# Performance work log

Hardware: AMD Instinct MI355X
Metric: run time of the kernel (lower is better)

Reference implementation:

```python
import jax, jax.numpy as jnp
import numpy as np

B, N, D = 4, 4096, 2048
E = D // 2  # inter_channels of the non-local block


def setup_inputs() -> dict:
    key = jax.random.key(0)
    ks = jax.random.split(key, 9)
    s_in = 1.0 / np.sqrt(D)   # conv1d(k=1) default init scale, fan_in=D
    s_e = 1.0 / np.sqrt(E)    # W conv: fan_in=E
    return {
        "images_feat": jax.random.normal(ks[0], (B, N, D), jnp.float32),
        "theta_w": jax.random.uniform(ks[1], (E, D), jnp.float32, -s_in, s_in),
        "theta_b": jax.random.uniform(ks[2], (E,), jnp.float32, -s_in, s_in),
        "phi_w": jax.random.uniform(ks[3], (E, D), jnp.float32, -s_in, s_in),
        "phi_b": jax.random.uniform(ks[4], (E,), jnp.float32, -s_in, s_in),
        "g_w": jax.random.uniform(ks[5], (E, D), jnp.float32, -s_in, s_in),
        "g_b": jax.random.uniform(ks[6], (E,), jnp.float32, -s_in, s_in),
        "W_w": jax.random.uniform(ks[7], (D, E), jnp.float32, -s_e, s_e),
        "W_b": jax.random.uniform(ks[8], (D,), jnp.float32, -s_e, s_e),
    }


def reference(images_feat, theta_w, theta_b, phi_w, phi_b, g_w, g_b, W_w, W_b):
    # Original: permute (B,N,D)->(B,D,N), apply 1x1 Conv1d projections (== linear
    # over the channel dim D), theta@phi^T -> softmax -> @g, W conv back, residual,
    # permute back. Expressed directly on (B,N,D).
    x = images_feat
    theta_x = jnp.einsum("bnd,ed->bne", x, theta_w) + theta_b  # (B,N,E)
    phi_x = jnp.einsum("bnd,ed->bne", x, phi_w) + phi_b        # (B,N,E)
    g_x = jnp.einsum("bnd,ed->bne", x, g_w) + g_b              # (B,N,E)
    f = jnp.einsum("bne,bme->bnm", theta_x, phi_x)             # (B,N,N)
    attn = jax.nn.softmax(f, axis=-1)
    y = jnp.einsum("bnm,bme->bne", attn, g_x)                  # (B,N,E)
    z = jnp.einsum("bne,de->bnd", y, W_w) + W_b + x            # residual, (B,N,D)
    return z
```

## Files before the change

### kernel.cpp

```cpp
#include <hip/hip_runtime.h>

typedef short bf16x8 __attribute__((ext_vector_type(8)));
typedef _Float16 f16x8 __attribute__((ext_vector_type(8)));
typedef float f32x4 __attribute__((ext_vector_type(4)));

__device__ __forceinline__ short f2h(float f) {
  _Float16 h = (_Float16)f;
  return __builtin_bit_cast(short, h);
}
__device__ __forceinline__ float h2f(short s) {
  return (float)__builtin_bit_cast(_Float16, s);
}

__device__ __forceinline__ void gload16(const void* g, void* lds) {
  __builtin_amdgcn_global_load_lds(
      (const __attribute__((address_space(1))) unsigned*)g,
      (__attribute__((address_space(3))) unsigned*)lds, 16, 0, 0);
}

template <int NF, int K, int OMODE, int BIAS_MODE, int RES>
__global__ __launch_bounds__(512, 2) void gemm256(
    const short* __restrict__ A, int lda, long sA,
    const short* __restrict__ B, int ldb, long sB,
    void* __restrict__ Cv, int ldc, long sC,
    const float* __restrict__ bias, const float* __restrict__ resid, long sR) {
  constexpr int BN = NF * 64;
  constexpr int BNB = BN * 128;
  constexpr int NT = K / 64;
  __shared__ char lds[65536 + 2 * BNB];

  A += (size_t)blockIdx.z * sA;
  B += (size_t)blockIdx.z * sB;
  char* Cb = (char*)Cv + (size_t)blockIdx.z * sC * (OMODE == 0 ? 4 : 2);
  const float* res = resid ? resid + (size_t)blockIdx.z * sR : nullptr;

  const int tid = threadIdx.x;
  const int wid = tid >> 6, lane = tid & 63;
  const int wr = wid >> 2, wc = wid & 3;
  const int fr = lane & 15, fq = lane >> 4;
  const size_t bm = (size_t)blockIdx.y * 256;
  const size_t bn = (size_t)blockIdx.x * BN;

  const int srow = wid * 8 + (lane >> 3);
  const int scolS = ((lane & 7) * 16) ^ ((srow & 7) << 4);
  const char* Ag = (const char*)A;
  const char* Bg = (const char*)B;

  const int swz = (fr & 7) << 4;
  int aoff[8], boff[NF];
#pragma unroll
  for (int m = 0; m < 8; m++)
    aoff[m] = (wr * 128 + m * 16 + fr) * 128 + ((fq * 16) ^ swz);
#pragma unroll
  for (int n = 0; n < NF; n++)
    boff[n] = (wc * NF * 16 + n * 16 + fr) * 128 + ((fq * 16) ^ swz);

  f32x4 acc[8][NF];
#pragma unroll
  for (int m = 0; m < 8; m++)
#pragma unroll
    for (int n = 0; n < NF; n++) acc[m][n] = (f32x4){0.f, 0.f, 0.f, 0.f};

  auto stage = [&](int t, int d) {
    const int ktb = t * 128;
#pragma unroll
    for (int c = 0; c < 4; ++c)
      gload16(Ag + ((size_t)(bm + c * 64 + srow) * lda) * 2 + ktb + scolS,
              &lds[d * 32768 + c * 8192 + wid * 1024]);
#pragma unroll
    for (int c = 0; c < NF; ++c)
      gload16(Bg + ((size_t)(bn + c * 64 + srow) * ldb) * 2 + ktb + scolS,
              &lds[65536 + d * BNB + c * 8192 + wid * 1024]);
  };

  stage(0, 0);
  int cur = 0;
#pragma unroll 2
  for (int t = 0; t < NT; ++t) {
    if (t + 1 < NT) stage(t + 1, cur ^ 1);
    __builtin_amdgcn_sched_barrier(0);
    if (t + 1 < NT) {
      if constexpr (NF == 4)
        asm volatile("s_waitcnt vmcnt(8)");
      else
        asm volatile("s_waitcnt vmcnt(6)");
    } else {
      asm volatile("s_waitcnt vmcnt(0)");
    }
    __builtin_amdgcn_sched_barrier(0);
    __builtin_amdgcn_s_barrier();
    __builtin_amdgcn_sched_barrier(0);
    {
      const int dA = cur * 32768, dB = 65536 + cur * BNB;
#pragma unroll
      for (int ks = 0; ks < 2; ++ks) {
        f16x8 ar[8], br[NF];
#pragma unroll
        for (int m = 0; m < 8; m++)
          ar[m] = *(const f16x8*)&lds[dA + (aoff[m] ^ (ks << 6))];
#pragma unroll
        for (int n = 0; n < NF; n++)
          br[n] = *(const f16x8*)&lds[dB + (boff[n] ^ (ks << 6))];
#pragma unroll
        for (int m = 0; m < 8; m++)
#pragma unroll
          for (int n = 0; n < NF; n++)
            acc[m][n] = __builtin_amdgcn_mfma_f32_16x16x32_f16(
                ar[m], br[n], acc[m][n], 0, 0, 0);
      }
    }
    __builtin_amdgcn_sched_barrier(0);
    __builtin_amdgcn_s_barrier();
    __builtin_amdgcn_sched_barrier(0);
    cur ^= 1;
  }

#pragma unroll
  for (int m = 0; m < 8; m++) {
    const size_t row0 = bm + wr * 128 + m * 16 + fq * 4;
#pragma unroll
    for (int n = 0; n < NF; n++) {
      const size_t col = bn + wc * NF * 16 + n * 16 + fr;
      float bcol = (BIAS_MODE == 1) ? bias[col] : 0.f;
#pragma unroll
      for (int r = 0; r < 4; r++) {
        float val = acc[m][n][r];
        const size_t row = row0 + r;
        const size_t idx = row * (size_t)ldc + col;
        if (BIAS_MODE == 1) val += bcol;
        if (BIAS_MODE == 2) val += bias[row];
        if (RES) val += res[idx];
        if (OMODE == 0)
          ((float*)Cb)[idx] = val;
        else
          ((short*)Cb)[idx] = f2h(val);
      }
    }
  }
}

__global__ __launch_bounds__(256) void cvt_f32_f16(const float* __restrict__ s,
                                                   short* __restrict__ d, int n) {
  int i = (blockIdx.x * 256 + threadIdx.x) * 8;
  if (i >= n) return;
  const float4 a = *(const float4*)(s + i);
  const float4 b = *(const float4*)(s + i + 4);
  bf16x8 o;
  o[0] = f2h(a.x); o[1] = f2h(a.y); o[2] = f2h(a.z); o[3] = f2h(a.w);
  o[4] = f2h(b.x); o[5] = f2h(b.y); o[6] = f2h(b.z); o[7] = f2h(b.w);
  *(bf16x8*)(d + i) = o;
}

__global__ __launch_bounds__(256) void softmax_rows(short* __restrict__ S) {
  const size_t row = blockIdx.x;
  short* rp = S + row * 4096;
  const int tid = threadIdx.x;
  const int lane = tid & 63, wid = tid >> 6;
  float v[16];
#pragma unroll
  for (int c = 0; c < 2; c++) {
    bf16x8 xv = *(const bf16x8*)(rp + (c * 256 + tid) * 8);
#pragma unroll
    for (int j = 0; j < 8; j++) v[c * 8 + j] = h2f(xv[j]);
  }
  float m = v[0];
#pragma unroll
  for (int i = 1; i < 16; i++) m = fmaxf(m, v[i]);
#pragma unroll
  for (int off = 32; off >= 1; off >>= 1) m = fmaxf(m, __shfl_xor(m, off));
  __shared__ float red[8];
  if (lane == 0) red[wid] = m;
  __syncthreads();
  m = fmaxf(fmaxf(red[0], red[1]), fmaxf(red[2], red[3]));
  float s = 0.f;
#pragma unroll
  for (int i = 0; i < 16; i++) {
    v[i] = __expf(v[i] - m);
    s += v[i];
  }
#pragma unroll
  for (int off = 32; off >= 1; off >>= 1) s += __shfl_xor(s, off);
  if (lane == 0) red[4 + wid] = s;
  __syncthreads();
  s = (red[4] + red[5]) + (red[6] + red[7]);
  const float rs = 1.0f / s;
#pragma unroll
  for (int c = 0; c < 2; c++) {
    bf16x8 o;
#pragma unroll
    for (int j = 0; j < 8; j++) o[j] = f2h(v[c * 8 + j] * rs);
    *(bf16x8*)(rp + (c * 256 + tid) * 8) = o;
  }
}

extern "C" void kernel_launch(void* const* d_in, const int* in_sizes, int n_in,
                              void* d_out, int out_size, void* d_ws,
                              size_t ws_size, hipStream_t stream) {
  const float* x   = (const float*)d_in[0];
  const float* thw = (const float*)d_in[1];
  const float* thb = (const float*)d_in[2];
  const float* phw = (const float*)d_in[3];
  const float* phb = (const float*)d_in[4];
  const float* gw  = (const float*)d_in[5];
  const float* gbi = (const float*)d_in[6];
  const float* Ww  = (const float*)d_in[7];
  const float* Wb  = (const float*)d_in[8];
  float* out = (float*)d_out;

  char* ws = (char*)d_ws;
  short* xf   = (short*)(ws);
  short* wcat = (short*)(ws + 67108864);
  short* gwb  = (short*)(ws + 75497472);
  short* wWb  = (short*)(ws + 79691776);
  float* bc   = (float*)(ws + 83886080);
  short* tpf  = (short*)(ws + 83894272);
  short* gT   = (short*)(ws + 151003136);
  short* sc   = (short*)(ws);

  cvt_f32_f16<<<16384, 256, 0, stream>>>(x, xf, 33554432);
  cvt_f32_f16<<<1024, 256, 0, stream>>>(thw, wcat, 2097152);
  cvt_f32_f16<<<1024, 256, 0, stream>>>(phw, wcat + 2097152, 2097152);
  cvt_f32_f16<<<1024, 256, 0, stream>>>(gw, gwb, 2097152);
  cvt_f32_f16<<<1024, 256, 0, stream>>>(Ww, wWb, 2097152);
  hipMemcpyAsync(bc, thb, 4096, hipMemcpyDeviceToDevice, stream);
  hipMemcpyAsync(bc + 1024, phb, 4096, hipMemcpyDeviceToDevice, stream);

  gemm256<4, 2048, 1, 1, 0><<<dim3(8, 64, 1), 512, 0, stream>>>(
      xf, 2048, 0L, wcat, 2048, 0L, tpf, 2048, 0L, bc, nullptr, 0L);

  gemm256<4, 2048, 1, 2, 0><<<dim3(16, 4, 4), 512, 0, stream>>>(
      gwb, 2048, 0L, xf, 2048, 8388608L, gT, 4096, 4194304L, gbi, nullptr, 0L);

  for (int p = 0; p < 2; ++p) {
    const short* tp = tpf + (size_t)p * 16777216;
    gemm256<4, 1024, 1, 0, 0><<<dim3(16, 16, 2), 512, 0, stream>>>(
        tp, 2048, 8388608L, tp + 1024, 2048, 8388608L,
        sc, 4096, 16777216L, nullptr, nullptr, 0L);
    softmax_rows<<<8192, 256, 0, stream>>>(sc);
    short* yp = tpf + (size_t)p * 16777216;
    gemm256<2, 4096, 1, 0, 0><<<dim3(8, 16, 2), 512, 0, stream>>>(
        sc, 4096, 16777216L, gT + (size_t)p * 8388608, 4096, 4194304L,
        yp, 1024, 4194304L, nullptr, nullptr, 0L);
    gemm256<4, 1024, 0, 1, 1><<<dim3(8, 16, 2), 512, 0, stream>>>(
        yp, 1024, 4194304L, wWb, 1024, 0L,
        out + (size_t)p * 16777216, 2048, 8388608L,
        Wb, x + (size_t)p * 16777216, 8388608L);
  }
}
```

Before: 716.9 us.

## Restructure GEMM mainloop into 4-slot LDS ring with prefetch distance two

```diff
diff --git a/kernel.cpp b/kernel.cpp
--- a/kernel.cpp
+++ b/kernel.cpp
@@ -19,15 +19,16 @@
 }
 
 template <int NF, int K, int OMODE, int BIAS_MODE, int RES>
-__global__ __launch_bounds__(512, 2) void gemm256(
+__global__ __launch_bounds__(512, 2) void gemmp(
     const short* __restrict__ A, int lda, long sA,
     const short* __restrict__ B, int ldb, long sB,
     void* __restrict__ Cv, int ldc, long sC,
     const float* __restrict__ bias, const float* __restrict__ resid, long sR) {
-  constexpr int BN = NF * 64;
-  constexpr int BNB = BN * 128;
-  constexpr int NT = K / 64;
-  __shared__ char lds[65536 + 2 * BNB];
+  constexpr int ACH = 16384;
+  constexpr int BCH = NF * 4096;
+  constexpr int CH = ACH + BCH;
+  constexpr int NP = K / 32;
+  __shared__ char lds[4 * CH];
 
   A += (size_t)blockIdx.z * sA;
   B += (size_t)blockIdx.z * sB;
@@ -39,21 +40,19 @@
   const int wr = wid >> 2, wc = wid & 3;
   const int fr = lane & 15, fq = lane >> 4;
   const size_t bm = (size_t)blockIdx.y * 256;
-  const size_t bn = (size_t)blockIdx.x * BN;
-
-  const int srow = wid * 8 + (lane >> 3);
-  const int scolS = ((lane & 7) * 16) ^ ((srow & 7) << 4);
+  const size_t bn = (size_t)blockIdx.x * (NF * 64);
+
   const char* Ag = (const char*)A;
   const char* Bg = (const char*)B;
 
-  const int swz = (fr & 7) << 4;
+  const int swz = (fr & 3) << 4;
   int aoff[8], boff[NF];
 #pragma unroll
   for (int m = 0; m < 8; m++)
-    aoff[m] = (wr * 128 + m * 16 + fr) * 128 + ((fq * 16) ^ swz);
+    aoff[m] = (wr * 128 + m * 16 + fr) * 64 + ((fq * 16) ^ swz);
 #pragma unroll
   for (int n = 0; n < NF; n++)
-    boff[n] = (wc * NF * 16 + n * 16 + fr) * 128 + ((fq * 16) ^ swz);
+    boff[n] = ACH + (wc * NF * 16 + n * 16 + fr) * 64 + ((fq * 16) ^ swz);
 
   f32x4 acc[8][NF];
 #pragma unroll
@@ -61,29 +60,47 @@
 #pragma unroll
     for (int n = 0; n < NF; n++) acc[m][n] = (f32x4){0.f, 0.f, 0.f, 0.f};
 
-  auto stage = [&](int t, int d) {
-    const int ktb = t * 128;
-#pragma unroll
-    for (int c = 0; c < 4; ++c)
-      gload16(Ag + ((size_t)(bm + c * 64 + srow) * lda) * 2 + ktb + scolS,
-              &lds[d * 32768 + c * 8192 + wid * 1024]);
-#pragma unroll
-    for (int c = 0; c < NF; ++c)
-      gload16(Bg + ((size_t)(bn + c * 64 + srow) * ldb) * 2 + ktb + scolS,
-              &lds[65536 + d * BNB + c * 8192 + wid * 1024]);
+  auto stage = [&](int p) {
+    char* s = &lds[(p & 3) * CH];
+    const int ktB = p * 64;
+#pragma unroll
+    for (int i = 0; i < 2; ++i) {
+      const int gi = (wid * 2 + i) * 64 + lane;
+      const int r = gi >> 2, c = gi & 3;
+      gload16(Ag + (size_t)(bm + r) * (size_t)(lda * 2) + ktB +
+                  ((c ^ (r & 3)) * 16),
+              s + (wid * 2 + i) * 1024);
+    }
+    if constexpr (NF == 4) {
+#pragma unroll
+      for (int i = 0; i < 2; ++i) {
+        const int gi = (wid * 2 + i) * 64 + lane;
+        const int r = gi >> 2, c = gi & 3;
+        gload16(Bg + (size_t)(bn + r) * (size_t)(ldb * 2) + ktB +
+                    ((c ^ (r & 3)) * 16),
+                s + ACH + (wid * 2 + i) * 1024);
+      }
+    } else {
+      const int gi = wid * 64 + lane;
+      const int r = gi >> 2, c = gi & 3;
+      gload16(Bg + (size_t)(bn + r) * (size_t)(ldb * 2) + ktB +
+                  ((c ^ (r & 3)) * 16),
+              s + ACH + wid * 1024);
+    }
   };
 
-  stage(0, 0);
-  int cur = 0;
-#pragma unroll 2
-  for (int t = 0; t < NT; ++t) {
-    if (t + 1 < NT) stage(t + 1, cur ^ 1);
-    __builtin_amdgcn_sched_barrier(0);
-    if (t + 1 < NT) {
-      if constexpr (NF == 4)
-        asm volatile("s_waitcnt vmcnt(8)");
-      else
-        asm volatile("s_waitcnt vmcnt(6)");
+  stage(0);
+  stage(1);
+#pragma unroll 4
+  for (int P = 0; P < NP; ++P) {
+    if (P + 2 < NP) stage(P + 2);
+    __builtin_amdgcn_sched_barrier(0);
+    if (P + 2 < NP) {
+      if constexpr (NF == 4) asm volatile("s_waitcnt vmcnt(8)");
+      else                   asm volatile("s_waitcnt vmcnt(6)");
+    } else if (P + 1 < NP) {
+      if constexpr (NF == 4) asm volatile("s_waitcnt vmcnt(4)");
+      else                   asm volatile("s_waitcnt vmcnt(3)");
     } else {
       asm volatile("s_waitcnt vmcnt(0)");
     }
@@ -91,28 +108,22 @@
     __builtin_amdgcn_s_barrier();
     __builtin_amdgcn_sched_barrier(0);
     {
-      const int dA = cur * 32768, dB = 65536 + cur * BNB;
-#pragma unroll
-      for (int ks = 0; ks < 2; ++ks) {
-        f16x8 ar[8], br[NF];
-#pragma unroll
-        for (int m = 0; m < 8; m++)
-          ar[m] = *(const f16x8*)&lds[dA + (aoff[m] ^ (ks << 6))];
+      const char* s = &lds[(P & 3) * CH];
+      f16x8 ar[8], br[NF];
+#pragma unroll
+      for (int m = 0; m < 8; m++) ar[m] = *(const f16x8*)(s + aoff[m]);
+#pragma unroll
+      for (int n = 0; n < NF; n++) br[n] = *(const f16x8*)(s + boff[n]);
+      __builtin_amdgcn_s_setprio(1);
+#pragma unroll
+      for (int m = 0; m < 8; m++)
 #pragma unroll
         for (int n = 0; n < NF; n++)
-          br[n] = *(const f16x8*)&lds[dB + (boff[n] ^ (ks << 6))];
-#pragma unroll
-        for (int m = 0; m < 8; m++)
-#pragma unroll
-          for (int n = 0; n < NF; n++)
-            acc[m][n] = __builtin_amdgcn_mfma_f32_16x16x32_f16(
-                ar[m], br[n], acc[m][n], 0, 0, 0);
-      }
-    }
-    __builtin_amdgcn_sched_barrier(0);
-    __builtin_amdgcn_s_barrier();
-    __builtin_amdgcn_sched_barrier(0);
-    cur ^= 1;
+          acc[m][n] = __builtin_amdgcn_mfma_f32_16x16x32_f16(ar[m], br[n],
+                                                             acc[m][n], 0, 0, 0);
+      __builtin_amdgcn_s_setprio(0);
+    }
+    __builtin_amdgcn_sched_barrier(0);
   }
 
 #pragma unroll
@@ -225,23 +236,23 @@
   hipMemcpyAsync(bc, thb, 4096, hipMemcpyDeviceToDevice, stream);
   hipMemcpyAsync(bc + 1024, phb, 4096, hipMemcpyDeviceToDevice, stream);
 
-  gemm256<4, 2048, 1, 1, 0><<<dim3(8, 64, 1), 512, 0, stream>>>(
+  gemmp<4, 2048, 1, 1, 0><<<dim3(8, 64, 1), 512, 0, stream>>>(
       xf, 2048, 0L, wcat, 2048, 0L, tpf, 2048, 0L, bc, nullptr, 0L);
 
-  gemm256<4, 2048, 1, 2, 0><<<dim3(16, 4, 4), 512, 0, stream>>>(
+  gemmp<4, 2048, 1, 2, 0><<<dim3(16, 4, 4), 512, 0, stream>>>(
       gwb, 2048, 0L, xf, 2048, 8388608L, gT, 4096, 4194304L, gbi, nullptr, 0L);
 
   for (int p = 0; p < 2; ++p) {
     const short* tp = tpf + (size_t)p * 16777216;
-    gemm256<4, 1024, 1, 0, 0><<<dim3(16, 16, 2), 512, 0, stream>>>(
+    gemmp<4, 1024, 1, 0, 0><<<dim3(16, 16, 2), 512, 0, stream>>>(
         tp, 2048, 8388608L, tp + 1024, 2048, 8388608L,
         sc, 4096, 16777216L, nullptr, nullptr, 0L);
     softmax_rows<<<8192, 256, 0, stream>>>(sc);
     short* yp = tpf + (size_t)p * 16777216;
-    gemm256<2, 4096, 1, 0, 0><<<dim3(8, 16, 2), 512, 0, stream>>>(
+    gemmp<2, 4096, 1, 0, 0><<<dim3(8, 16, 2), 512, 0, stream>>>(
         sc, 4096, 16777216L, gT + (size_t)p * 8388608, 4096, 4194304L,
         yp, 1024, 4194304L, nullptr, nullptr, 0L);
-    gemm256<4, 1024, 0, 1, 1><<<dim3(8, 16, 2), 512, 0, stream>>>(
+    gemmp<4, 1024, 0, 1, 1><<<dim3(8, 16, 2), 512, 0, stream>>>(
         yp, 1024, 4194304L, wWb, 1024, 0L,
         out + (size_t)p * 16777216, 2048, 8388608L,
         Wb, x + (size_t)p * 16777216, 8388608L);
```

Result: slower. 762.7 us (+6.4%).

## Replace GEMM with 256x256-tile, 4-wave kernel using 128-entry per-wave accumulators

Applied to the files above, without the earlier changes.

```diff
diff --git a/kernel.cpp b/kernel.cpp
--- a/kernel.cpp
+++ b/kernel.cpp
@@ -18,16 +18,14 @@
       (__attribute__((address_space(3))) unsigned*)lds, 16, 0, 0);
 }
 
-template <int NF, int K, int OMODE, int BIAS_MODE, int RES>
-__global__ __launch_bounds__(512, 2) void gemm256(
+template <int K, int OMODE, int BIAS_MODE, int RES>
+__global__ __launch_bounds__(256, 1) void gemmf(
     const short* __restrict__ A, int lda, long sA,
     const short* __restrict__ B, int ldb, long sB,
     void* __restrict__ Cv, int ldc, long sC,
     const float* __restrict__ bias, const float* __restrict__ resid, long sR) {
-  constexpr int BN = NF * 64;
-  constexpr int BNB = BN * 128;
   constexpr int NT = K / 64;
-  __shared__ char lds[65536 + 2 * BNB];
+  __shared__ __align__(1024) char lds[131072];
 
   A += (size_t)blockIdx.z * sA;
   B += (size_t)blockIdx.z * sB;
@@ -36,91 +34,98 @@
 
   const int tid = threadIdx.x;
   const int wid = tid >> 6, lane = tid & 63;
-  const int wr = wid >> 2, wc = wid & 3;
+  const int wm = wid >> 1, wn = wid & 1;
   const int fr = lane & 15, fq = lane >> 4;
   const size_t bm = (size_t)blockIdx.y * 256;
-  const size_t bn = (size_t)blockIdx.x * BN;
-
-  const int srow = wid * 8 + (lane >> 3);
-  const int scolS = ((lane & 7) * 16) ^ ((srow & 7) << 4);
+  const size_t bn = (size_t)blockIdx.x * 256;
+
   const char* Ag = (const char*)A;
   const char* Bg = (const char*)B;
+  const size_t ldaB = (size_t)lda * 2, ldbB = (size_t)ldb * 2;
+
+  const int lrow = lane >> 3;
+  const int scol = ((lane & 7) ^ lrow) * 16;
 
   const int swz = (fr & 7) << 4;
-  int aoff[8], boff[NF];
+  const int aoff0 = (wm * 128 + fr) * 128 + ((fq * 16) ^ swz);
+  const int boff0 = 32768 + (wn * 128 + fr) * 128 + ((fq * 16) ^ swz);
+
+  f32x4 acc[8][8];
 #pragma unroll
   for (int m = 0; m < 8; m++)
-    aoff[m] = (wr * 128 + m * 16 + fr) * 128 + ((fq * 16) ^ swz);
-#pragma unroll
-  for (int n = 0; n < NF; n++)
-    boff[n] = (wc * NF * 16 + n * 16 + fr) * 128 + ((fq * 16) ^ swz);
-
-  f32x4 acc[8][NF];
-#pragma unroll
-  for (int m = 0; m < 8; m++)
-#pragma unroll
-    for (int n = 0; n < NF; n++) acc[m][n] = (f32x4){0.f, 0.f, 0.f, 0.f};
-
-  auto stage = [&](int t, int d) {
-    const int ktb = t * 128;
-#pragma unroll
-    for (int c = 0; c < 4; ++c)
-      gload16(Ag + ((size_t)(bm + c * 64 + srow) * lda) * 2 + ktb + scolS,
-              &lds[d * 32768 + c * 8192 + wid * 1024]);
-#pragma unroll
-    for (int c = 0; c < NF; ++c)
-      gload16(Bg + ((size_t)(bn + c * 64 + srow) * ldb) * 2 + ktb + scolS,
-              &lds[65536 + d * BNB + c * 8192 + wid * 1024]);
+#pragma unroll
+    for (int n = 0; n < 8; n++) acc[m][n] = (f32x4){0.f, 0.f, 0.f, 0.f};
+
+  auto stage = [&](int t) {
+    char* s = &lds[(t & 1) * 65536];
+    const size_t ktB = (size_t)t * 128;
+#pragma unroll
+    for (int i = 0; i < 8; ++i)
+      gload16(Ag + (bm + 32 * i + wid * 8 + lrow) * ldaB + ktB + scol,
+              s + i * 4096 + wid * 1024);
+#pragma unroll
+    for (int i = 0; i < 8; ++i)
+      gload16(Bg + (bn + 32 * i + wid * 8 + lrow) * ldbB + ktB + scol,
+              s + 32768 + i * 4096 + wid * 1024);
   };
 
-  stage(0, 0);
-  int cur = 0;
-#pragma unroll 2
+  stage(0);
   for (int t = 0; t < NT; ++t) {
-    if (t + 1 < NT) stage(t + 1, cur ^ 1);
+    __builtin_amdgcn_s_barrier();
     __builtin_amdgcn_sched_barrier(0);
     if (t + 1 < NT) {
-      if constexpr (NF == 4)
-        asm volatile("s_waitcnt vmcnt(8)");
-      else
-        asm volatile("s_waitcnt vmcnt(6)");
+      stage(t + 1);
+      __builtin_amdgcn_sched_barrier(0);
+      asm volatile("s_waitcnt vmcnt(16)");
     } else {
       asm volatile("s_waitcnt vmcnt(0)");
     }
     __builtin_amdgcn_sched_barrier(0);
-    __builtin_amdgcn_s_barrier();
-    __builtin_amdgcn_sched_barrier(0);
-    {
-      const int dA = cur * 32768, dB = 65536 + cur * BNB;
-#pragma unroll
-      for (int ks = 0; ks < 2; ++ks) {
-        f16x8 ar[8], br[NF];
-#pragma unroll
-        for (int m = 0; m < 8; m++)
-          ar[m] = *(const f16x8*)&lds[dA + (aoff[m] ^ (ks << 6))];
-#pragma unroll
-        for (int n = 0; n < NF; n++)
-          br[n] = *(const f16x8*)&lds[dB + (boff[n] ^ (ks << 6))];
-#pragma unroll
-        for (int m = 0; m < 8; m++)
-#pragma unroll
-          for (int n = 0; n < NF; n++)
-            acc[m][n] = __builtin_amdgcn_mfma_f32_16x16x32_f16(
-                ar[m], br[n], acc[m][n], 0, 0, 0);
-      }
-    }
-    __builtin_amdgcn_sched_barrier(0);
-    __builtin_amdgcn_s_barrier();
-    __builtin_amdgcn_sched_barrier(0);
-    cur ^= 1;
+    const char* s = &lds[(t & 1) * 65536];
+    f16x8 a0[8], b0[8], a1[8], b1[8];
+#pragma unroll
+    for (int m = 0; m < 8; m++)
+      a0[m] = *(const f16x8*)(s + (aoff0 + m * 2048));
+#pragma unroll
+    for (int n = 0; n < 8; n++)
+      b0[n] = *(const f16x8*)(s + (boff0 + n * 2048));
+#pragma unroll
+    for (int m = 0; m < 8; m++)
+      a1[m] = *(const f16x8*)(s + ((aoff0 ^ 64) + m * 2048));
+#pragma unroll
+    for (int n = 0; n < 8; n++)
+      b1[n] = *(const f16x8*)(s + ((boff0 ^ 64) + n * 2048));
+    __builtin_amdgcn_sched_barrier(0);
+    asm volatile("s_waitcnt lgkmcnt(15)");
+    __builtin_amdgcn_sched_barrier(0);
+    __builtin_amdgcn_s_setprio(1);
+#pragma unroll
+    for (int m = 0; m < 8; m++)
+#pragma unroll
+      for (int n = 0; n < 8; n++)
+        acc[m][n] = __builtin_amdgcn_mfma_f32_16x16x32_f16(a0[m], b0[n],
+                                                           acc[m][n], 0, 0, 0);
+    __builtin_amdgcn_s_setprio(0);
+    __builtin_amdgcn_sched_barrier(0);
+    asm volatile("s_waitcnt lgkmcnt(0)");
+    __builtin_amdgcn_sched_barrier(0);
+    __builtin_amdgcn_s_setprio(1);
+#pragma unroll
+    for (int m = 0; m < 8; m++)
+#pragma unroll
+      for (int n = 0; n < 8; n++)
+        acc[m][n] = __builtin_amdgcn_mfma_f32_16x16x32_f16(a1[m], b1[n],
+                                                           acc[m][n], 0, 0, 0);
+    __builtin_amdgcn_s_setprio(0);
+    __builtin_amdgcn_sched_barrier(0);
   }
 
 #pragma unroll
   for (int m = 0; m < 8; m++) {
-    const size_t row0 = bm + wr * 128 + m * 16 + fq * 4;
-#pragma unroll
-    for (int n = 0; n < NF; n++) {
-      const size_t col = bn + wc * NF * 16 + n * 16 + fr;
+    const size_t row0 = bm + wm * 128 + m * 16 + fq * 4;
+#pragma unroll
+    for (int n = 0; n < 8; n++) {
+      const size_t col = bn + wn * 128 + n * 16 + fr;
       float bcol = (BIAS_MODE == 1) ? bias[col] : 0.f;
 #pragma unroll
       for (int r = 0; r < 4; r++) {
@@ -225,23 +230,23 @@
   hipMemcpyAsync(bc, thb, 4096, hipMemcpyDeviceToDevice, stream);
   hipMemcpyAsync(bc + 1024, phb, 4096, hipMemcpyDeviceToDevice, stream);
 
-  gemm256<4, 2048, 1, 1, 0><<<dim3(8, 64, 1), 512, 0, stream>>>(
+  gemmf<2048, 1, 1, 0><<<dim3(8, 64, 1), 256, 0, stream>>>(
       xf, 2048, 0L, wcat, 2048, 0L, tpf, 2048, 0L, bc, nullptr, 0L);
 
-  gemm256<4, 2048, 1, 2, 0><<<dim3(16, 4, 4), 512, 0, stream>>>(
+  gemmf<2048, 1, 2, 0><<<dim3(16, 4, 4), 256, 0, stream>>>(
       gwb, 2048, 0L, xf, 2048, 8388608L, gT, 4096, 4194304L, gbi, nullptr, 0L);
 
   for (int p = 0; p < 2; ++p) {
     const short* tp = tpf + (size_t)p * 16777216;
-    gemm256<4, 1024, 1, 0, 0><<<dim3(16, 16, 2), 512, 0, stream>>>(
+    gemmf<1024, 1, 0, 0><<<dim3(16, 16, 2), 256, 0, stream>>>(
         tp, 2048, 8388608L, tp + 1024, 2048, 8388608L,
         sc, 4096, 16777216L, nullptr, nullptr, 0L);
     softmax_rows<<<8192, 256, 0, stream>>>(sc);
     short* yp = tpf + (size_t)p * 16777216;
-    gemm256<2, 4096, 1, 0, 0><<<dim3(8, 16, 2), 512, 0, stream>>>(
+    gemmf<4096, 1, 0, 0><<<dim3(4, 16, 2), 256, 0, stream>>>(
         sc, 4096, 16777216L, gT + (size_t)p * 8388608, 4096, 4194304L,
         yp, 1024, 4194304L, nullptr, nullptr, 0L);
-    gemm256<4, 1024, 0, 1, 1><<<dim3(8, 16, 2), 512, 0, stream>>>(
+    gemmf<1024, 0, 1, 1><<<dim3(8, 16, 2), 256, 0, stream>>>(
         yp, 1024, 4194304L, wWb, 1024, 0L,
         out + (size_t)p * 16777216, 2048, 8388608L,
         Wb, x + (size_t)p * 16777216, 8388608L);
```

Measured after the change: 761.2 us. 1.06x slower.
